# Optimization experiments

Measured on AMD Instinct MI355X. Metric: run time of the kernel, lower is better.

The kernel has to match this reference:

```python
import jax, jax.numpy as jnp
import numpy as np

B, S, D, H = 4, 1024, 1024, 16
HD = D // H  # per-head dim = 64
NEG = -10000000000.0


def setup_inputs() -> dict:
    key = jax.random.key(0)
    ks = jax.random.split(key, 12)
    q = jax.random.normal(ks[0], (B, S, D), jnp.float32)
    k = jax.random.normal(ks[1], (B, S, D), jnp.float32)
    v = jax.random.normal(ks[2], (B, S, D), jnp.float32)
    mask = jax.random.randint(ks[3], (B, S, S), 0, 2).astype(jnp.int32)
    sc = 1.0 / np.sqrt(D)
    Wq = jax.random.normal(ks[4], (H, D, HD), jnp.float32) * sc
    bq = jnp.zeros((H, HD), jnp.float32)
    Wk = jax.random.normal(ks[5], (H, D, HD), jnp.float32) * sc
    bk = jnp.zeros((H, HD), jnp.float32)
    Wv = jax.random.normal(ks[6], (H, D, HD), jnp.float32) * sc
    bv = jnp.zeros((H, HD), jnp.float32)
    Wo = jax.random.normal(ks[7], (D, D), jnp.float32) * sc
    bo = jnp.zeros((D,), jnp.float32)
    return {"query": q, "key": k, "value": v, "attention_mask": mask,
            "Wq": Wq, "bq": bq, "Wk": Wk, "bk": bk, "Wv": Wv, "bv": bv,
            "Wo": Wo, "bo": bo}


def reference(query, key, value, attention_mask, Wq, bq, Wk, bk, Wv, bv, Wo, bo):
    # batched per-head projections: [B,S,D] x [H,D,E] -> [B,H,S,E]
    q = jnp.einsum('bsd,hde->bhse', query, Wq) + bq[None, :, None, :]
    k = jnp.einsum('bsd,hde->bhse', key, Wk) + bk[None, :, None, :]
    v = jnp.einsum('bsd,hde->bhse', value, Wv) + bv[None, :, None, :]
    # NOTE: scale uses key_dim (model_size = full D), faithful to source
    score = jnp.einsum('bhse,bhte->bhst', q, k) / jnp.sqrt(jnp.float32(D))
    m = attention_mask.astype(jnp.float32)[:, None, :, :]  # [B,1,S,S]
    score = score + (1.0 - m) * NEG
    attn = jax.nn.softmax(score, axis=-1) * m  # double masking
    heads = jnp.einsum('bhst,bhte->bhse', attn, v)  # [B,H,S,E]
    # concat heads along feature dim (head order preserved)
    heads = heads.transpose(0, 2, 1, 3).reshape(B, S, D)
    return heads @ Wo + bo
```

## Files before the change

### kernel.cpp

```cpp
#include <hip/hip_runtime.h>

#define B_ 4
#define S_ 1024
#define D_ 1024
#define H_ 16
#define E_ 64
#define BS_ (B_*S_)
#define BHSE_ (B_*H_*S_*E_)

typedef __attribute__((ext_vector_type(8))) short bf16x8;
typedef __attribute__((ext_vector_type(4))) float f32x4;
typedef __attribute__((ext_vector_type(4))) unsigned int u32x4;

__device__ __forceinline__ unsigned short f2bf(float f) {
    unsigned int x = __float_as_uint(f);
    x = (x + 0x7FFFu + ((x >> 16) & 1u)) >> 16;
    return (unsigned short)x;
}
__device__ __forceinline__ float bf2f(unsigned short u) {
    return __uint_as_float(((unsigned int)u) << 16);
}
__device__ __forceinline__ float ldin(const void* p, size_t i, int isb) {
    return isb ? bf2f(((const unsigned short*)p)[i]) : ((const float*)p)[i];
}

__device__ __forceinline__ unsigned int cvtpk(float lo, float hi) {
    unsigned int r;
    asm("v_cvt_pk_bf16_f32 %0, %1, %2" : "=v"(r) : "v"(lo), "v"(hi));
    return r;
}
__device__ __forceinline__ unsigned int bperm(int srclane4, unsigned int v) {
    return (unsigned int)__builtin_amdgcn_ds_bpermute(srclane4, (int)v);
}
__device__ __forceinline__ bf16x8 u4bf(u32x4 w) {
    union { u32x4 u; bf16x8 h; } c; c.u = w; return c.h;
}

#if __has_builtin(__builtin_amdgcn_exp2f)
#define EXP2(x) __builtin_amdgcn_exp2f(x)
#else
#define EXP2(x) __expf((x) * 0.6931471805599453f)
#endif

__device__ __forceinline__ void gl2lds16(const void* g, void* l) {
    __builtin_amdgcn_global_load_lds(
        (const __attribute__((address_space(1))) void*)g,
        (__attribute__((address_space(3))) void*)l, 16, 0, 0);
}

__device__ __forceinline__ int detect_isb(const unsigned int* q) {
    unsigned int wv = q[threadIdx.x & 63];
    unsigned int lo = wv & 0xFFFFu;
    unsigned int e = (lo >> 7) & 0xFFu;
    int ok = (lo == 0u) || (e >= 100u && e <= 145u);
    return __popcll(__ballot(ok)) >= 48;
}

__global__ __launch_bounds__(256) void preproc(
        const void* q_, const void* k_, const void* v_, const int* mask,
        const void* Wq, const void* Wk, const void* Wv, const void* Wo,
        const void* bq_, const void* bk_, const void* bv_, const void* bo_,
        unsigned short* WT, float* biases, unsigned long long* packT,
        unsigned short* Aconv) {
    __shared__ unsigned short Tt[64][72];
    const int isb = detect_isb((const unsigned int*)q_);
    const int blk = blockIdx.x, t = threadIdx.x;

    if (blk < 1024) {
        const int c0 = blk & 15, r0 = ((blk >> 4) & 15) * 64, z = blk >> 8;
        const void* src = (z == 0) ? Wq : (z == 1) ? Wk : (z == 2) ? Wv : Wo;
        {
            int dl = t >> 2, qc = t & 3;
            size_t base;
            if (z < 3) base = (size_t)c0 * 65536 + (size_t)(r0 + dl) * 64 + qc * 16;
            else       base = (size_t)(r0 + dl) * 1024 + (size_t)c0 * 64 + qc * 16;
            if (isb) {
                const unsigned short* s = (const unsigned short*)src + base;
                bf16x8 a0 = *(const bf16x8*)s, a1 = *(const bf16x8*)(s + 8);
#pragma unroll
                for (int j = 0; j < 8; j++) {
                    Tt[qc * 16 + j][dl] = (unsigned short)a0[j];
                    Tt[qc * 16 + 8 + j][dl] = (unsigned short)a1[j];
                }
            } else {
                const float* s = (const float*)src + base;
#pragma unroll
                for (int j = 0; j < 16; j++) Tt[qc * 16 + j][dl] = f2bf(s[j]);
            }
        }
        __syncthreads();
        {
            int el = t >> 2, qc = t & 3;
            size_t dst = (size_t)z * D_ * D_ + (size_t)(c0 * 64 + el) * D_ + r0 + qc * 16;
            *(bf16x8*)&WT[dst]     = *(const bf16x8*)&Tt[el][qc * 16];
            *(bf16x8*)&WT[dst + 8] = *(const bf16x8*)&Tt[el][qc * 16 + 8];
        }
        if (z == 3 && ((blk >> 4) & 15) == 0 && c0 < 4) {
            const void* bs = (c0 == 0) ? bq_ : (c0 == 1) ? bk_
                           : (c0 == 2) ? bv_ : bo_;
#pragma unroll
            for (int j = 0; j < 4; j++) {
                int i = t * 4 + j;
                biases[c0 * 1024 + i] = ldin(bs, i, isb);
            }
        }
    } else if (blk < 5120) {
        int unit = (blk - 1024) * 4 + (t >> 6);
        int lane = t & 63;
        int b = unit >> 12, rem = unit & 4095, s0 = (rem >> 4) * 4, kt = rem & 15;
        const int* mb = mask + ((size_t)b * 1024 + s0) * 1024 + kt * 64 + lane;
        unsigned long long bits[4];
#pragma unroll
        for (int j = 0; j < 4; j++) bits[j] = __ballot(mb[j * 1024] != 0);
        if (lane < 4) {
            unsigned long long bb = (lane == 0) ? bits[0] : (lane == 1) ? bits[1]
                                  : (lane == 2) ? bits[2] : bits[3];
            packT[((size_t)b * 16 + kt) * 1024 + s0 + lane] = bb;
        }
    } else {
        if (isb) return;
        int blk2 = blk - 5120;
        const int z = blk2 >> 11;
        const float* s = (z == 0) ? (const float*)q_ : (z == 1) ? (const float*)k_
                                                                : (const float*)v_;
        const size_t i = ((size_t)(blk2 & 2047) * 256 + t) * 8;
        f32x4 a0 = *(const f32x4*)(s + i);
        f32x4 a1 = *(const f32x4*)(s + i + 4);
        bf16x8 o;
#pragma unroll
        for (int j = 0; j < 4; j++) {
            o[j]     = (short)f2bf(a0[j]);
            o[4 + j] = (short)f2bf(a1[j]);
        }
        *(bf16x8*)&Aconv[(size_t)z * ((size_t)BS_ * D_) + i] = o;
    }
}

template<int BM, int BN, int MODE, int MINW>
__global__ __launch_bounds__(256, MINW) void gemm_k(
        const void* A0, const void* A1, const void* A2, const unsigned short* Aconv,
        const unsigned short* BtB, const float* biasB, void* dstB,
        const unsigned int* qdet) {
    constexpr int TOT16 = (BM + BN) * 32;
    constexpr int CALLS = TOT16 / 512;
    constexpr int CPW = CALLS / 4;
    constexpr int MT = BM / 32;
    constexpr int NT = BN / 32;
    __shared__ unsigned short buf[2][TOT16];

    const int fl = detect_isb(qdet);
    const int t = threadIdx.x, lane = t & 63, w = t >> 6;
    const int lm = lane & 15, q4 = lane >> 4;
    const int wm = w >> 1, wn = w & 1;
    const int lr = lane >> 2;
    const int ls = lane & 3;
    const int lg = ls ^ ((lr >> 1) & 3);

    const unsigned short* Abf;
    const unsigned short* Bt;
    const float* bias;
    int z = 0, m0, n0, phase;
    if (MODE == 0) {
        int bid = blockIdx.x + gridDim.x * (blockIdx.y + gridDim.y * blockIdx.z);
        int xcd = bid & 7, idx = bid >> 3;
        z = idx >> 5;
        int r = idx & 31;
        int mt = (xcd << 2) + (r & 3);
        int nt = r >> 2;
        m0 = mt * BM; n0 = nt * BN;
        phase = (nt * 13 + z * 5) & 31;
        const void* Ain = (z == 0) ? A0 : (z == 1 ? A1 : A2);
        Abf = fl ? (const unsigned short*)Ain
                 : Aconv + (size_t)z * ((size_t)BS_ * D_);
        Bt = BtB + (size_t)z * D_ * D_;
        bias = biasB + z * 1024;
    } else {
        Abf = (const unsigned short*)A0;
        Bt = BtB; bias = biasB;
        int bid = blockIdx.x + (blockIdx.y << 5);
        int xcd = bid & 7, idx = bid >> 3;
        m0 = ((xcd << 2) + (idx & 3)) * BM;
        n0 = (idx >> 2) * BN;
        phase = ((idx >> 2) * 13) & 31;
    }

    auto stage = [&](int kk, int bi) {
#pragma unroll
        for (int i = 0; i < CPW; ++i) {
            int c = w * CPW + i;
            int row = c * 16 + lr;
            const unsigned short* g;
            if (row < BM)
                g = Abf + (size_t)(m0 + row) * D_ + kk + lg * 8;
            else
                g = Bt + (size_t)(n0 + row - BM) * D_ + kk + lg * 8;
            gl2lds16(g, &buf[bi][c * 512]);
        }
    };

    f32x4 acc[MT][NT];
#pragma unroll
    for (int i = 0; i < MT; i++)
#pragma unroll
        for (int j = 0; j < NT; j++) acc[i][j] = (f32x4){0.f, 0.f, 0.f, 0.f};

    stage((phase & 31) * 32, 0);
    for (int it = 0; it < D_ / 32; ++it) {
        const int bi = it & 1;
        __syncthreads();
        if (it < D_ / 32 - 1) stage(((it + 1 + phase) & 31) * 32, bi ^ 1);

        const unsigned short* As = buf[bi];
        const unsigned short* Bs = buf[bi] + BM * 32;
        bf16x8 af[MT], bv[NT];
#pragma unroll
        for (int mt = 0; mt < MT; mt++) {
            int row = wm * (BM / 2) + mt * 16 + lm;
            af[mt] = *(const bf16x8*)&As[row * 32 + (q4 ^ ((row >> 1) & 3)) * 8];
        }
#pragma unroll
        for (int nt = 0; nt < NT; nt++) {
            int row = wn * (BN / 2) + nt * 16 + lm;
            bv[nt] = *(const bf16x8*)&Bs[row * 32 + (q4 ^ ((row >> 1) & 3)) * 8];
        }
#pragma unroll
        for (int mt = 0; mt < MT; mt++)
#pragma unroll
            for (int nt = 0; nt < NT; nt++)
                acc[mt][nt] = __builtin_amdgcn_mfma_f32_16x16x32_bf16(
                    af[mt], bv[nt], acc[mt][nt], 0, 0, 0);
    }

#pragma unroll
    for (int mt = 0; mt < MT; mt++)
#pragma unroll
        for (int nt = 0; nt < NT; nt++) {
            int N = n0 + wn * (BN / 2) + nt * 16 + lm;
            int Mb = m0 + wm * (BM / 2) + mt * 16 + q4 * 4;
            if (MODE == 0 && z == 2) {
                int bb = Mb >> 10, sb = Mb & 1023, hh = N >> 6, e = N & 63;
                unsigned long long hv = 0;
#pragma unroll
                for (int r = 0; r < 4; r++)
                    hv |= (unsigned long long)f2bf(acc[mt][nt][r] + bias[N]) << (16 * r);
                unsigned short* d16 = (unsigned short*)dstB + (size_t)2 * BHSE_;
                *(unsigned long long*)&d16[(((size_t)(bb * H_ + hh) * E_ + e) << 10) + sb] = hv;
            } else {
#pragma unroll
                for (int r = 0; r < 4; r++) {
                    int M = Mb + r;
                    float v = acc[mt][nt][r] + bias[N];
                    if (MODE == 0) {
                        int bb = M >> 10, s = M & 1023, hh = N >> 6, e = N & 63;
                        unsigned short* d16 = (unsigned short*)dstB + (size_t)z * BHSE_;
                        d16[((size_t)(bb * H_ + hh) * S_ + s) * E_ + e] = f2bf(v);
                    } else {
                        size_t idx = (size_t)M * D_ + N;
                        if (fl) ((unsigned short*)dstB)[idx] = f2bf(v);
                        else    ((float*)dstB)[idx] = v;
                    }
                }
            }
        }
}

__global__ __launch_bounds__(512, 2) void attn64(
        const unsigned short* Qp, const unsigned short* Kp, const unsigned short* VpT,
        const unsigned long long* packT, unsigned short* heads) {
    __shared__ unsigned short KT[2][4096];
    __shared__ unsigned short VT[2][4096];

    const int bid = blockIdx.x + (blockIdx.y << 3) + (blockIdx.z << 7);
    const int xcd = bid & 7, idx = bid >> 3;
    const int qt = idx >> 3;
    const int hb = xcd * 8 + (idx & 7);
    const int h = hb & 15, b = hb >> 4;

    const int t = threadIdx.x, w = t >> 6, lane = t & 63, lm = lane & 15, q4 = lane >> 4;
    const size_t bh = ((size_t)b * H_ + h) * S_ * E_;
    const unsigned short* Qb = Qp + bh;
    const unsigned short* Kb = Kp + bh;
    const unsigned short* Vb = VpT + bh;
    const int q0 = qt * 128 + w * 16;

    const int l3 = lane >> 3, l7 = lane & 7;
    const int kLaneOff = l3 * 64 + (l7 ^ l3) * 8;
    const int vLaneOff = l3 * 1024 + (l7 ^ l3) * 8;

    const int sw = lm & 7;
    const int c0 = (q4 ^ sw) * 8, c1 = ((q4 ^ 4) ^ sw) * 8;

    const int srcA4 = ((lane & 15) | ((lane & 16) << 1)) << 2;
    const int srcB4 = srcA4 + 64;
    const bool selHi = (lane & 32) != 0;

    bf16x8 bq0 = *(const bf16x8*)&Qb[(size_t)(q0 + lm) * E_ + q4 * 8];
    bf16x8 bq1 = *(const bf16x8*)&Qb[(size_t)(q0 + lm) * E_ + 32 + q4 * 8];

    f32x4 oacc[4];
#pragma unroll
    for (int i = 0; i < 4; i++) oacc[i] = (f32x4){0.f, 0.f, 0.f, 0.f};
    float mrun = -3.0e38f, lrun = 0.f;
    const float scale2 = 0.03125f * 1.4426950408889634f;

#define STAGE(ktile, bufi)                                                    \
    {                                                                         \
        int k0s = (ktile) * 64;                                               \
        _Pragma("unroll")                                                     \
        for (int i_ = 0; i_ < 2; ++i_) {                                      \
            int c_ = w * 2 + i_;                                              \
            if (c_ < 8) {                                                     \
                gl2lds16(Kb + (size_t)k0s * 64 + c_ * 512 + kLaneOff,         \
                         &KT[bufi][c_ * 512]);                                \
            } else {                                                          \
                int cc_ = c_ - 8;                                             \
                gl2lds16(Vb + (size_t)cc_ * 8192 + k0s + vLaneOff,            \
                         &VT[bufi][cc_ * 512]);                               \
            }                                                                 \
        }                                                                     \
    }

    STAGE(0, 0)
    unsigned long long mk = packT[(size_t)b * 16 * 1024 + q0 + lm];

    for (int kt = 0; kt < S_ / 64; ++kt) {
        const int bufi = kt & 1;
        __syncthreads();
        unsigned long long mknext = 0;
        if (kt < 15) {
            STAGE(kt + 1, bufi ^ 1)
            mknext = packT[((size_t)b * 16 + kt + 1) * 1024 + q0 + lm];
        }

        f32x4 st[4];
#pragma unroll
        for (int jt = 0; jt < 4; ++jt) {
            const unsigned short* kr = &KT[bufi][(jt * 16 + lm) * 64];
            bf16x8 ka0 = *(const bf16x8*)&kr[c0];
            bf16x8 ka1 = *(const bf16x8*)&kr[c1];
            f32x4 zz = (f32x4){0.f, 0.f, 0.f, 0.f};
            zz = __builtin_amdgcn_mfma_f32_16x16x32_bf16(ka0, bq0, zz, 0, 0, 0);
            zz = __builtin_amdgcn_mfma_f32_16x16x32_bf16(ka1, bq1, zz, 0, 0, 0);
            st[jt] = zz;
        }

        float mx0 = fmaxf(fmaxf(st[0][0], st[0][1]), fmaxf(st[0][2], st[0][3]));
        float mx1 = fmaxf(fmaxf(st[1][0], st[1][1]), fmaxf(st[1][2], st[1][3]));
        float mx2 = fmaxf(fmaxf(st[2][0], st[2][1]), fmaxf(st[2][2], st[2][3]));
        float mx3 = fmaxf(fmaxf(st[3][0], st[3][1]), fmaxf(st[3][2], st[3][3]));
        float tmx = fmaxf(fmaxf(mx0, mx1), fmaxf(mx2, mx3));
        tmx = fmaxf(tmx, __shfl_xor(tmx, 16, 64));
        tmx = fmaxf(tmx, __shfl_xor(tmx, 32, 64));
        float pmax = tmx * scale2;

        if (!__all(pmax - mrun <= 8.f)) {
            float mnew = fmaxf(mrun, pmax);
            float alpha = EXP2(mrun - mnew);
            lrun *= alpha;
#pragma unroll
            for (int nt = 0; nt < 4; nt++) oacc[nt] = oacc[nt] * alpha;
            mrun = mnew;
        }
        const float mneg = -mrun;

        unsigned int mn = (unsigned int)(mk >> (q4 * 4));
        unsigned int mh = (unsigned int)(mk >> (q4 * 4 + 32));

        float ssum = 0.f;
        unsigned int cl[8];
#pragma unroll
        for (int jt = 0; jt < 4; ++jt) {
            unsigned int mm = (jt & 2) ? mh : mn;
            const int sh = (jt & 1) * 16;
            float p0 = EXP2(fmaf(st[jt][0], scale2, mneg));
            float p1 = EXP2(fmaf(st[jt][1], scale2, mneg));
            float p2 = EXP2(fmaf(st[jt][2], scale2, mneg));
            float p3 = EXP2(fmaf(st[jt][3], scale2, mneg));
            p0 = (mm & (1u << (sh + 0))) ? p0 : 0.f;
            p1 = (mm & (1u << (sh + 1))) ? p1 : 0.f;
            p2 = (mm & (1u << (sh + 2))) ? p2 : 0.f;
            p3 = (mm & (1u << (sh + 3))) ? p3 : 0.f;
            ssum += (p0 + p1) + (p2 + p3);
            cl[jt * 2]     = cvtpk(p0, p1);
            cl[jt * 2 + 1] = cvtpk(p2, p3);
        }
        ssum += __shfl_xor(ssum, 16, 64);
        ssum += __shfl_xor(ssum, 32, 64);
        lrun += ssum;

        u32x4 w0, w1;
        {
            unsigned int aA0 = bperm(srcA4, cl[0]), aA2 = bperm(srcA4, cl[2]);
            unsigned int aA1 = bperm(srcA4, cl[1]), aA3 = bperm(srcA4, cl[3]);
            unsigned int aB0 = bperm(srcB4, cl[0]), aB2 = bperm(srcB4, cl[2]);
            unsigned int aB1 = bperm(srcB4, cl[1]), aB3 = bperm(srcB4, cl[3]);
            w0 = (u32x4){selHi ? aA2 : aA0, selHi ? aA3 : aA1,
                         selHi ? aB2 : aB0, selHi ? aB3 : aB1};
            unsigned int bA0 = bperm(srcA4, cl[4]), bA2 = bperm(srcA4, cl[6]);
            unsigned int bA1 = bperm(srcA4, cl[5]), bA3 = bperm(srcA4, cl[7]);
            unsigned int bB0 = bperm(srcB4, cl[4]), bB2 = bperm(srcB4, cl[6]);
            unsigned int bB1 = bperm(srcB4, cl[5]), bB3 = bperm(srcB4, cl[7]);
            w1 = (u32x4){selHi ? bA2 : bA0, selHi ? bA3 : bA1,
                         selHi ? bB2 : bB0, selHi ? bB3 : bB1};
        }
        bf16x8 bp0 = u4bf(w0);
        bf16x8 bp1 = u4bf(w1);

#pragma unroll
        for (int nt = 0; nt < 4; nt++) {
            const unsigned short* vr = &VT[bufi][(nt * 16 + lm) * 64];
            bf16x8 va0 = *(const bf16x8*)&vr[c0];
            bf16x8 va1 = *(const bf16x8*)&vr[c1];
            oacc[nt] = __builtin_amdgcn_mfma_f32_16x16x32_bf16(va0, bp0, oacc[nt], 0, 0, 0);
            oacc[nt] = __builtin_amdgcn_mfma_f32_16x16x32_bf16(va1, bp1, oacc[nt], 0, 0, 0);
        }
        mk = mknext;
    }

    float inv = 1.0f / lrun;
#pragma unroll
    for (int nt = 0; nt < 4; nt++) {
        unsigned int lo = cvtpk(oacc[nt][0] * inv, oacc[nt][1] * inv);
        unsigned int hi = cvtpk(oacc[nt][2] * inv, oacc[nt][3] * inv);
        unsigned long long hv = (unsigned long long)lo | ((unsigned long long)hi << 32);
        *(unsigned long long*)&heads[(size_t)(b * S_ + q0 + lm) * D_ + h * E_ + nt * 16 + q4 * 4] = hv;
    }
}

extern "C" void kernel_launch(void* const* d_in, const int* in_sizes, int n_in,
                              void* d_out, int out_size, void* d_ws, size_t ws_size,
                              hipStream_t stream) {
    char* ws = (char*)d_ws;
    unsigned short* WT = (unsigned short*)(ws + 256);
    unsigned short* WqT = WT;
    unsigned short* WoT = WT + (size_t)3 * D_ * D_;
    float* biases = (float*)(WT + (size_t)4 * D_ * D_);
    float* bq = biases;
    float* bo = biases + 3 * 1024;
    unsigned short* Qp = (unsigned short*)(biases + 4 * 1024);
    unsigned short* Kp = Qp + (size_t)BHSE_;
    unsigned short* Vp = Kp + (size_t)BHSE_;
    unsigned short* heads = Vp + (size_t)BHSE_;
    unsigned long long* packT = (unsigned long long*)(heads + (size_t)BHSE_);
    unsigned short* Aconv = (unsigned short*)(packT + (size_t)B_ * 16 * S_);

    preproc<<<11264, 256, 0, stream>>>(
        d_in[0], d_in[1], d_in[2], (const int*)d_in[3],
        d_in[4], d_in[6], d_in[8], d_in[10],
        d_in[5], d_in[7], d_in[9], d_in[11],
        WT, biases, packT, Aconv);
    gemm_k<128, 128, 0, 3><<<dim3(32, 8, 3), 256, 0, stream>>>(
        d_in[0], d_in[1], d_in[2], Aconv, WqT, bq, Qp,
        (const unsigned int*)d_in[0]);
    attn64<<<dim3(8, 16, 4), 512, 0, stream>>>(Qp, Kp, Vp, packT, heads);
    gemm_k<128, 64, 1, 4><<<dim3(32, 16, 1), 256, 0, stream>>>(
        heads, nullptr, nullptr, nullptr, WoT, bo, d_out,
        (const unsigned int*)d_in[0]);
}
```

Before: 225.8 us.

## Software-pipeline QK^T with triple-buffered K/V and compute row sums via MFMA

Restructures the attention loop so the QK^T MFMAs for the next key tile run while the current tile's softmax and PV run. K/V staging moves to a triple-buffered LDS ring with rotating pointers, prefetching two tiles ahead. The softmax denominator is now an MFMA against a vector of ones instead of scalar adds and cross-lane shuffles, and launch bounds ask for higher occupancy. The cost is more LDS and more live registers for the extra score tile, which may conflict with the higher occupancy request. Row sums now come from bf16-rounded probabilities, which slightly changes numerics.

Result: no change. 226.0 us (+0.1%).

```diff
diff --git a/kernel.cpp b/kernel.cpp
--- a/kernel.cpp
+++ b/kernel.cpp
@@ -264,11 +264,11 @@
         }
 }
 
-__global__ __launch_bounds__(512, 2) void attn64(
+__global__ __launch_bounds__(512, 4) void attn64(
         const unsigned short* Qp, const unsigned short* Kp, const unsigned short* VpT,
         const unsigned long long* packT, unsigned short* heads) {
-    __shared__ unsigned short KT[2][4096];
-    __shared__ unsigned short VT[2][4096];
+    __shared__ unsigned short KT[3][4096];
+    __shared__ unsigned short VT[3][4096];
 
     const int bid = blockIdx.x + (blockIdx.y << 3) + (blockIdx.z << 7);
     const int xcd = bid & 7, idx = bid >> 3;
@@ -297,13 +297,18 @@
     bf16x8 bq0 = *(const bf16x8*)&Qb[(size_t)(q0 + lm) * E_ + q4 * 8];
     bf16x8 bq1 = *(const bf16x8*)&Qb[(size_t)(q0 + lm) * E_ + 32 + q4 * 8];
 
+    bf16x8 ones;
+#pragma unroll
+    for (int j = 0; j < 8; j++) ones[j] = (short)0x3F80;
+
     f32x4 oacc[4];
 #pragma unroll
     for (int i = 0; i < 4; i++) oacc[i] = (f32x4){0.f, 0.f, 0.f, 0.f};
-    float mrun = -3.0e38f, lrun = 0.f;
+    f32x4 accL = (f32x4){0.f, 0.f, 0.f, 0.f};
+    float mrun = -3.0e38f;
     const float scale2 = 0.03125f * 1.4426950408889634f;
 
-#define STAGE(ktile, bufi)                                                    \
+#define STAGE(ktile, kdst, vdst)                                              \
     {                                                                         \
         int k0s = (ktile) * 64;                                               \
         _Pragma("unroll")                                                     \
@@ -311,31 +316,19 @@
             int c_ = w * 2 + i_;                                              \
             if (c_ < 8) {                                                     \
                 gl2lds16(Kb + (size_t)k0s * 64 + c_ * 512 + kLaneOff,         \
-                         &KT[bufi][c_ * 512]);                                \
+                         (kdst) + c_ * 512);                                  \
             } else {                                                          \
                 int cc_ = c_ - 8;                                             \
                 gl2lds16(Vb + (size_t)cc_ * 8192 + k0s + vLaneOff,            \
-                         &VT[bufi][cc_ * 512]);                               \
+                         (vdst) + cc_ * 512);                                 \
             }                                                                 \
         }                                                                     \
     }
 
-    STAGE(0, 0)
-    unsigned long long mk = packT[(size_t)b * 16 * 1024 + q0 + lm];
-
-    for (int kt = 0; kt < S_ / 64; ++kt) {
-        const int bufi = kt & 1;
-        __syncthreads();
-        unsigned long long mknext = 0;
-        if (kt < 15) {
-            STAGE(kt + 1, bufi ^ 1)
-            mknext = packT[((size_t)b * 16 + kt + 1) * 1024 + q0 + lm];
-        }
-
-        f32x4 st[4];
+    auto QK = [&](const unsigned short* kb, f32x4* st) {
 #pragma unroll
         for (int jt = 0; jt < 4; ++jt) {
-            const unsigned short* kr = &KT[bufi][(jt * 16 + lm) * 64];
+            const unsigned short* kr = &kb[(jt * 16 + lm) * 64];
             bf16x8 ka0 = *(const bf16x8*)&kr[c0];
             bf16x8 ka1 = *(const bf16x8*)&kr[c1];
             f32x4 zz = (f32x4){0.f, 0.f, 0.f, 0.f};
@@ -343,11 +336,29 @@
             zz = __builtin_amdgcn_mfma_f32_16x16x32_bf16(ka1, bq1, zz, 0, 0, 0);
             st[jt] = zz;
         }
-
-        float mx0 = fmaxf(fmaxf(st[0][0], st[0][1]), fmaxf(st[0][2], st[0][3]));
-        float mx1 = fmaxf(fmaxf(st[1][0], st[1][1]), fmaxf(st[1][2], st[1][3]));
-        float mx2 = fmaxf(fmaxf(st[2][0], st[2][1]), fmaxf(st[2][2], st[2][3]));
-        float mx3 = fmaxf(fmaxf(st[3][0], st[3][1]), fmaxf(st[3][2], st[3][3]));
+    };
+
+    unsigned short *kA = &KT[0][0], *kB = &KT[1][0], *kC = &KT[2][0];
+    unsigned short *vA = &VT[0][0], *vB = &VT[1][0], *vC = &VT[2][0];
+
+    STAGE(0, kA, vA)
+    STAGE(1, kB, vB)
+    unsigned long long mk = packT[(size_t)b * 16 * 1024 + q0 + lm];
+    __syncthreads();
+    f32x4 stC[4], stN[4];
+    QK(kA, stC);
+
+    for (int kt = 0; kt < S_ / 64; ++kt) {
+        __syncthreads();
+        unsigned long long mknext = 0;
+        if (kt < 15) mknext = packT[((size_t)b * 16 + kt + 1) * 1024 + q0 + lm];
+        if (kt < 14) STAGE(kt + 2, kC, vC)
+        if (kt < 15) QK(kB, stN);
+
+        float mx0 = fmaxf(fmaxf(stC[0][0], stC[0][1]), fmaxf(stC[0][2], stC[0][3]));
+        float mx1 = fmaxf(fmaxf(stC[1][0], stC[1][1]), fmaxf(stC[1][2], stC[1][3]));
+        float mx2 = fmaxf(fmaxf(stC[2][0], stC[2][1]), fmaxf(stC[2][2], stC[2][3]));
+        float mx3 = fmaxf(fmaxf(stC[3][0], stC[3][1]), fmaxf(stC[3][2], stC[3][3]));
         float tmx = fmaxf(fmaxf(mx0, mx1), fmaxf(mx2, mx3));
         tmx = fmaxf(tmx, __shfl_xor(tmx, 16, 64));
         tmx = fmaxf(tmx, __shfl_xor(tmx, 32, 64));
@@ -356,7 +367,7 @@
         if (!__all(pmax - mrun <= 8.f)) {
             float mnew = fmaxf(mrun, pmax);
             float alpha = EXP2(mrun - mnew);
-            lrun *= alpha;
+            accL = accL * alpha;
 #pragma unroll
             for (int nt = 0; nt < 4; nt++) oacc[nt] = oacc[nt] * alpha;
             mrun = mnew;
@@ -366,27 +377,22 @@
         unsigned int mn = (unsigned int)(mk >> (q4 * 4));
         unsigned int mh = (unsigned int)(mk >> (q4 * 4 + 32));
 
-        float ssum = 0.f;
         unsigned int cl[8];
 #pragma unroll
         for (int jt = 0; jt < 4; ++jt) {
             unsigned int mm = (jt & 2) ? mh : mn;
             const int sh = (jt & 1) * 16;
-            float p0 = EXP2(fmaf(st[jt][0], scale2, mneg));
-            float p1 = EXP2(fmaf(st[jt][1], scale2, mneg));
-            float p2 = EXP2(fmaf(st[jt][2], scale2, mneg));
-            float p3 = EXP2(fmaf(st[jt][3], scale2, mneg));
+            float p0 = EXP2(fmaf(stC[jt][0], scale2, mneg));
+            float p1 = EXP2(fmaf(stC[jt][1], scale2, mneg));
+            float p2 = EXP2(fmaf(stC[jt][2], scale2, mneg));
+            float p3 = EXP2(fmaf(stC[jt][3], scale2, mneg));
             p0 = (mm & (1u << (sh + 0))) ? p0 : 0.f;
             p1 = (mm & (1u << (sh + 1))) ? p1 : 0.f;
             p2 = (mm & (1u << (sh + 2))) ? p2 : 0.f;
             p3 = (mm & (1u << (sh + 3))) ? p3 : 0.f;
-            ssum += (p0 + p1) + (p2 + p3);
             cl[jt * 2]     = cvtpk(p0, p1);
             cl[jt * 2 + 1] = cvtpk(p2, p3);
         }
-        ssum += __shfl_xor(ssum, 16, 64);
-        ssum += __shfl_xor(ssum, 32, 64);
-        lrun += ssum;
 
         u32x4 w0, w1;
         {
@@ -406,18 +412,28 @@
         bf16x8 bp0 = u4bf(w0);
         bf16x8 bp1 = u4bf(w1);
 
+        accL = __builtin_amdgcn_mfma_f32_16x16x32_bf16(ones, bp0, accL, 0, 0, 0);
+        accL = __builtin_amdgcn_mfma_f32_16x16x32_bf16(ones, bp1, accL, 0, 0, 0);
+
 #pragma unroll
         for (int nt = 0; nt < 4; nt++) {
-            const unsigned short* vr = &VT[bufi][(nt * 16 + lm) * 64];
+            const unsigned short* vr = &vA[(nt * 16 + lm) * 64];
             bf16x8 va0 = *(const bf16x8*)&vr[c0];
             bf16x8 va1 = *(const bf16x8*)&vr[c1];
             oacc[nt] = __builtin_amdgcn_mfma_f32_16x16x32_bf16(va0, bp0, oacc[nt], 0, 0, 0);
             oacc[nt] = __builtin_amdgcn_mfma_f32_16x16x32_bf16(va1, bp1, oacc[nt], 0, 0, 0);
         }
+
+        unsigned short* tp;
+        tp = kA; kA = kB; kB = kC; kC = tp;
+        tp = vA; vA = vB; vB = vC; vC = tp;
+        if (kt < 15) {
+            stC[0] = stN[0]; stC[1] = stN[1]; stC[2] = stN[2]; stC[3] = stN[3];
+        }
         mk = mknext;
     }
 
-    float inv = 1.0f / lrun;
+    float inv = 1.0f / accL[0];
 #pragma unroll
     for (int nt = 0; nt < 4; nt++) {
         unsigned int lo = cvtpk(oacc[nt][0] * inv, oacc[nt][1] * inv);
```
